# Kernel tuning notes

Measured on AMD Instinct MI355X. Metric: run time of the kernel, lower is better.

Reference implementation:

```python
import jax, jax.numpy as jnp
import numpy as np

SHAPES = ((96, 144), (48, 72), (24, 36), (12, 18))
BS, EMBED = 2, 256
HEADS, LEVELS, POINTS = 8, 4, 4
NEMBED = EMBED // HEADS
LEN_V = sum(h * w for h, w in SHAPES)
LEN_Q = LEN_V  # encoder self-attention: every pixel is a query


def _pos_grid_init():
    # Faithful re-implementation of MultiScaleDeformableAttention.pos_grid_init
    thetas = jnp.arange(HEADS, dtype=jnp.float32) * (2.0 * np.pi / HEADS)
    g = jnp.stack([jnp.cos(thetas), jnp.sin(thetas)], -1)
    g = g / jnp.max(jnp.abs(g), axis=-1, keepdims=True)
    g = jnp.tile(g.reshape(HEADS, 1, 1, 2), (1, LEVELS, POINTS, 1))
    scale = (jnp.arange(POINTS, dtype=jnp.float32) + 1.0)[None, None, :, None]
    return g * scale  # [HEADS, LEVELS, POINTS, 2]


def setup_inputs() -> dict:
    ks = jax.random.split(jax.random.key(0), 7)
    return {
        'query': jax.random.normal(ks[0], (BS, LEN_Q, EMBED), jnp.float32),
        'ref_points': jax.random.uniform(ks[1], (BS, LEN_Q, LEVELS, 2), jnp.float32),
        'value': jax.random.normal(ks[2], (BS, LEN_V, EMBED), jnp.float32),
        'pad_mask': jnp.ones((BS, LEN_V), dtype=bool),
        'value_proj_kernel': jax.random.normal(ks[3], (EMBED, HEADS, NEMBED), jnp.float32) * 0.05,
        'value_proj_bias': jnp.zeros((HEADS, NEMBED), jnp.float32),
        'sampling_offsets_kernel': jax.random.normal(ks[4], (EMBED, HEADS, LEVELS, POINTS, 2), jnp.float32) * 0.01,
        'sampling_offsets_bias': _pos_grid_init(),
        'attn_kernel': jax.random.normal(ks[5], (EMBED, HEADS, LEVELS * POINTS), jnp.float32) * 0.02,
        'attn_bias': jnp.zeros((HEADS, LEVELS * POINTS), jnp.float32),
        'out_kernel': jax.random.normal(ks[6], (HEADS, NEMBED, EMBED), jnp.float32) * 0.05,
        'out_bias': jnp.zeros((EMBED,), jnp.float32),
        'train': 0,
    }


def _bilinear(im, grid, w, h):
    """Batched 2D bilinear interpolation, zero outside the image.

    im:   [B, h*w, e] flattened feature map
    grid: [B, N, 2] normalized coords (pixel centers at (x+0.5)/w, (y+0.5)/h)
    Returns [B, N, e]. Identical math to the original gather-based kernel:
    out-of-bounds corner weights are zeroed, so zero-padding the image by 1
    reproduces the 'empty'-pad + masked-weight scheme exactly.
    """
    B, _, e = im.shape
    imp = jnp.pad(im.reshape(B, h, w, e), ((0, 0), (1, 1), (1, 1), (0, 0)))
    imp = imp.reshape(B, (h + 2) * (w + 2), e)
    x = grid[..., 0] * w - 0.5
    y = grid[..., 1] * h - 0.5
    x0 = jnp.floor(x).astype(jnp.int32)
    y0 = jnp.floor(y).astype(jnp.int32)
    x1 = x0 + 1
    y1 = y0 + 1

    def gather(yy, xx):
        idx = jnp.clip(yy + 1, 0, h + 1) * (w + 2) + jnp.clip(xx + 1, 0, w + 1)
        return jnp.take_along_axis(imp, idx[..., None], axis=1)  # [B, N, e]

    x0f, y0f = x0.astype(x.dtype), y0.astype(y.dtype)
    x1f, y1f = x1.astype(x.dtype), y1.astype(y.dtype)
    inx0 = (x0 >= 0) & (x0 <= w - 1)
    inx1 = (x1 >= 0) & (x1 <= w - 1)
    iny0 = (y0 >= 0) & (y0 <= h - 1)
    iny1 = (y1 >= 0) & (y1 <= h - 1)
    wa = jnp.where(inx0 & iny0, (x1f - x) * (y1f - y), 0.0)
    wb = jnp.where(inx0 & iny1, (x1f - x) * (y - y0f), 0.0)
    wc = jnp.where(inx1 & iny0, (x - x0f) * (y1f - y), 0.0)
    wd = jnp.where(inx1 & iny1, (x - x0f) * (y - y0f), 0.0)
    return (gather(y0, x0) * wa[..., None] + gather(y1, x0) * wb[..., None]
            + gather(y0, x1) * wc[..., None] + gather(y1, x1) * wd[..., None])


def _forward(query, ref_points, value, pad_mask, vpk, vpb, sok, sob, ak, ab, okern, obias):
    bs, len_q, _ = query.shape
    len_v = value.shape[1]
    # value projection + pad masking -> [bs*H, len_v, nembed]
    v = jnp.einsum('bve,ehd->bvhd', value, vpk) + vpb
    v = jnp.where(pad_mask[..., None, None], v, 0)
    v = v.transpose(0, 2, 1, 3).reshape(bs * HEADS, len_v, NEMBED)
    # sampling locations (ref_dim == 2 branch) -> [bs*H, L, P*len_q, 2]
    off = jnp.einsum('bqe,ehlpc->bqhlpc', query, sok) + sob
    offset_norm = jnp.array([[w, h] for h, w in SHAPES], dtype=query.dtype)  # [L, 2]
    loc = ref_points[:, :, None, :, None, :] + off / offset_norm[None, None, None, :, None, :]
    loc = loc.transpose(0, 2, 3, 4, 1, 5).reshape(bs * HEADS, LEVELS, POINTS * len_q, 2)
    # attention weights (softmax over L*P) -> [bs*H, len_q, L*P]
    aw = jnp.einsum('bqe,ehm->bqhm', query, ak) + ab
    aw = jax.nn.softmax(aw, axis=-1)
    aw = aw.transpose(0, 2, 1, 3).reshape(bs * HEADS, len_q, LEVELS * POINTS)
    # per-level bilinear sampling, concatenated level-major over (level, point)
    starts = np.cumsum([0] + [h * w for h, w in SHAPES])
    sampled = []
    for li, (h, w) in enumerate(SHAPES):
        vl = v[:, starts[li]:starts[li + 1], :]
        s = _bilinear(vl, loc[:, li], w, h)  # [bs*H, P*len_q, nembed]
        sampled.append(s.reshape(bs * HEADS, POINTS, len_q, NEMBED))
    sampled = jnp.concatenate(sampled, axis=1)  # [bs*H, L*P, len_q, nembed]
    x = jnp.einsum('blqe,bql->bqe', sampled, aw)
    x = x.reshape(bs, HEADS, len_q, NEMBED)
    # output projection: DenseGeneral over (heads, nembed)
    return jnp.einsum('bhqe,hed->bqd', x, okern) + obias


def reference(query, ref_points, value, pad_mask, value_proj_kernel, value_proj_bias,
              sampling_offsets_kernel, sampling_offsets_bias, attn_kernel, attn_bias,
              out_kernel, out_bias, train):
    del train  # eval mode (no remat); math is identical
    return _forward(query, ref_points, value, pad_mask, value_proj_kernel, value_proj_bias,
                    sampling_offsets_kernel, sampling_offsets_bias, attn_kernel, attn_bias,
                    out_kernel, out_bias)
```

## Files before the change

### kernel.cpp

```cpp
#include <hip/hip_runtime.h>
#include <math.h>

#define LEN 18360
#define M_ROWS (2 * LEN)
#define NTASK (16 * LEN)

typedef unsigned short u16;
typedef __attribute__((ext_vector_type(8))) short bf16x8;
typedef __attribute__((ext_vector_type(4))) float f32x4;

__device__ __forceinline__ u16 f2bf(float f) {
  unsigned u = __float_as_uint(f);
  return (u16)((u + 0x7fffu + ((u >> 16) & 1u)) >> 16);
}
__device__ __forceinline__ void async_cp16(const void* g, void* l) {
  __builtin_amdgcn_global_load_lds(
      (const __attribute__((address_space(1))) unsigned*)g,
      (__attribute__((address_space(3))) unsigned*)l, 16, 0, 0);
}

__global__ __launch_bounds__(256) void gemm_mfma_k(
    const u16* __restrict__ A0, const u16* __restrict__ Bt0,
    const float* __restrict__ bias0, void* __restrict__ C0, int N0, int nt0,
    int mode0, int split, const u16* __restrict__ A1,
    const u16* __restrict__ Bt1, const float* __restrict__ bias1,
    void* __restrict__ C1, int N1, int nt1, int mode1) {
  __shared__ u16 A_lds[8 * 512];
  __shared__ u16 B_lds[8 * 512];

  int bid = (int)blockIdx.x;
  const u16* A;
  const u16* Bt;
  const float* bias;
  void* Cv;
  int N, nt, mode;
  if (bid < split) {
    A = A0; Bt = Bt0; bias = bias0; Cv = C0; N = N0; nt = nt0; mode = mode0;
  } else {
    bid -= split;
    A = A1; Bt = Bt1; bias = bias1; Cv = C1; N = N1; nt = nt1; mode = mode1;
  }
  const int n0 = (bid % nt) << 7;
  const int m0 = (bid / nt) << 7;

  const int tid = threadIdx.x;
  const int w = tid >> 6;
  const int lane = tid & 63;
  const int wm = w & 1, wn = w >> 1;
  const int mr = lane & 15;
  const int kq = (lane >> 4) * 8;

  f32x4 acc[4][4];
#pragma unroll
  for (int i = 0; i < 4; i++)
#pragma unroll
    for (int j = 0; j < 4; j++) acc[i][j] = (f32x4){0.f, 0.f, 0.f, 0.f};

  for (int k0 = 0; k0 < 256; k0 += 32) {
    __syncthreads();
#pragma unroll
    for (int t = 0; t < 2; t++) {
      const int st = 2 * w + t;
      const int ga = min(m0 + st * 16 + mr, M_ROWS - 1);
      async_cp16(A + (size_t)ga * 256 + k0 + kq, &A_lds[st * 512]);
      const int gb = n0 + st * 16 + mr;
      async_cp16(Bt + (size_t)gb * 256 + k0 + kq, &B_lds[st * 512]);
    }
    __syncthreads();

    bf16x8 af[4], bf[4];
#pragma unroll
    for (int i = 0; i < 4; i++)
      af[i] = *(const bf16x8*)&A_lds[(wm * 4 + i) * 512 + lane * 8];
#pragma unroll
    for (int j = 0; j < 4; j++)
      bf[j] = *(const bf16x8*)&B_lds[(wn * 4 + j) * 512 + lane * 8];
#pragma unroll
    for (int i = 0; i < 4; i++)
#pragma unroll
      for (int j = 0; j < 4; j++)
        acc[i][j] = __builtin_amdgcn_mfma_f32_16x16x32_bf16(bf[j], af[i],
                                                            acc[i][j], 0, 0, 0);
  }

#pragma unroll
  for (int i = 0; i < 4; i++) {
    const int row = m0 + wm * 64 + i * 16 + mr;
    if (row >= M_ROWS) continue;
#pragma unroll
    for (int j = 0; j < 4; j++) {
      const int col = n0 + wn * 64 + j * 16 + (lane >> 4) * 4;
      const float4 b4 = *(const float4*)(bias + col);
      float4 o;
      o.x = acc[i][j][0] + b4.x;
      o.y = acc[i][j][1] + b4.y;
      o.z = acc[i][j][2] + b4.z;
      o.w = acc[i][j][3] + b4.w;
      if (mode == 0) {
        *(float4*)((float*)Cv + (size_t)row * N + col) = o;
      } else if (mode == 1) {
        const int b = row >= LEN;
        const int lv = row - b * LEN;
        const int h = col >> 5, d = col & 31;
        uint2 p;
        p.x = (unsigned)f2bf(o.x) | ((unsigned)f2bf(o.y) << 16);
        p.y = (unsigned)f2bf(o.z) | ((unsigned)f2bf(o.w) << 16);
        *(uint2*)((u16*)Cv + ((size_t)((b * 8 + h) * LEN + lv)) * 32 + d) = p;
      } else {
        uint2 p;
        p.x = (unsigned)f2bf(o.x) | ((unsigned)f2bf(o.y) << 16);
        p.y = (unsigned)f2bf(o.z) | ((unsigned)f2bf(o.w) << 16);
        *(uint2*)((u16*)Cv + (size_t)row * N + col) = p;
      }
    }
  }
}

__global__ __launch_bounds__(256) void cast_qv_k(const float* __restrict__ q,
                                                 const float* __restrict__ v,
                                                 u16* __restrict__ qb,
                                                 u16* __restrict__ vb) {
  const size_t i = ((size_t)blockIdx.x * 256 + threadIdx.x) * 4;
  float4 a = *(const float4*)(q + i);
  uint2 p;
  p.x = (unsigned)f2bf(a.x) | ((unsigned)f2bf(a.y) << 16);
  p.y = (unsigned)f2bf(a.z) | ((unsigned)f2bf(a.w) << 16);
  *(uint2*)&qb[i] = p;
  float4 c = *(const float4*)(v + i);
  p.x = (unsigned)f2bf(c.x) | ((unsigned)f2bf(c.y) << 16);
  p.y = (unsigned)f2bf(c.z) | ((unsigned)f2bf(c.w) << 16);
  *(uint2*)&vb[i] = p;
}

__global__ __launch_bounds__(256) void wcast_k(
    const float* __restrict__ vpk, const float* __restrict__ sok,
    const float* __restrict__ ak, const float* __restrict__ ok,
    const float* __restrict__ sob, const float* __restrict__ ab,
    u16* __restrict__ vpk_t, u16* __restrict__ sa_t, u16* __restrict__ ok_t,
    float* __restrict__ bias_cat) {
  const int gid = blockIdx.x * 256 + threadIdx.x;
  if (gid < 65536) {
    const int d = gid, n = d >> 8, k = d & 255;
    vpk_t[d] = f2bf(vpk[k * 256 + n]);
  } else if (gid < 131072) {
    const int d = gid - 65536, n = d >> 8, k = d & 255;
    sa_t[d] = f2bf(sok[k * 256 + n]);
  } else if (gid < 163840) {
    const int d = gid - 131072, n = d >> 8, k = d & 255;
    sa_t[65536 + d] = f2bf(ak[k * 128 + n]);
  } else if (gid < 229376) {
    const int d = gid - 163840, n = d >> 8, k = d & 255;
    ok_t[d] = f2bf(ok[k * 256 + n]);
  } else if (gid < 229760) {
    const int d = gid - 229376;
    bias_cat[d] = (d < 256) ? sob[d] : ab[d - 256];
  }
}

__global__ __launch_bounds__(256) void sampler_k(
    const u16* __restrict__ v,
    const u16* __restrict__ offaw,
    const float* __restrict__ refp,
    u16* __restrict__ xb)
{
  __shared__ int2 meta[4][258];
  const int tid = threadIdx.x;

  const int cW[4] = {144, 72, 36, 18};
  const int cH[4] = {96, 48, 24, 12};
  const int cS[4] = {0, 13824, 17280, 18144};

  {
    const int t = tid >> 4;
    const int s = tid & 15;
    const int l = s >> 2;

    const int task = (blockIdx.x << 4) + t;
    const int q = task % LEN;
    const int bh = task / LEN;
    const int h = bh & 7;
    const int b = bh >> 3;
    const size_t qrow = (size_t)(b * LEN + q);
    const u16* rowp = offaw + qrow * 384;

    const float logit = __uint_as_float((unsigned)rowp[256 + h * 16 + s] << 16);
    float mx = logit;
#pragma unroll
    for (int m = 1; m < 16; m <<= 1) mx = fmaxf(mx, __shfl_xor(mx, m, 16));
    const float e = __expf(logit - mx);
    float ssum = e;
#pragma unroll
    for (int m = 1; m < 16; m <<= 1) ssum += __shfl_xor(ssum, m, 16);
    const float wsm = e / ssum;

    const int W = cW[l], H = cH[l], ST = cS[l];
    const float2 rp = ((const float2*)(refp + qrow * 8))[l];
    const unsigned upair = ((const unsigned*)(rowp + h * 32))[s];
    const float ox = __uint_as_float(upair << 16);
    const float oy = __uint_as_float(upair & 0xffff0000u);
    const float X = rp.x * (float)W + ox - 0.5f;
    const float Y = rp.y * (float)H + oy - 0.5f;
    const float fx = floorf(X), fy = floorf(Y);
    const int x0 = (int)fx, y0 = (int)fy;
    const float dx = X - fx, dy = Y - fy;
    const float ux = 1.f - dx, uy = 1.f - dy;
    const bool bx0 = (unsigned)x0 < (unsigned)W;
    const bool bx1 = (unsigned)(x0 + 1) < (unsigned)W;
    const bool by0 = (unsigned)y0 < (unsigned)H;
    const bool by1 = (unsigned)(y0 + 1) < (unsigned)H;
    const int xc0 = min(max(x0, 0), W - 1);
    const int xc1 = min(max(x0 + 1, 0), W - 1);
    const int yc0 = min(max(y0, 0), H - 1);
    const int yc1 = min(max(y0 + 1, 0), H - 1);
    const float w00 = (bx0 & by0) ? wsm * ux * uy : 0.f;
    const float w10 = (bx1 & by0) ? wsm * dx * uy : 0.f;
    const float w01 = (bx0 & by1) ? wsm * ux * dy : 0.f;
    const float w11 = (bx1 & by1) ? wsm * dx * dy : 0.f;

    meta[0][tid] = make_int2((ST + yc0 * W + xc0) << 6, __float_as_int(w00));
    meta[1][tid] = make_int2((ST + yc0 * W + xc1) << 6, __float_as_int(w10));
    meta[2][tid] = make_int2((ST + yc1 * W + xc0) << 6, __float_as_int(w01));
    meta[3][tid] = make_int2((ST + yc1 * W + xc1) << 6, __float_as_int(w11));
  }
  __syncthreads();

  const int u = tid >> 5;
  const int lane = tid & 31;
  const int c = lane >> 3;
  const int dq = lane & 7;

#pragma unroll
  for (int rep = 0; rep < 2; rep++) {
    const int t = u + rep * 8;
    const int task = (blockIdx.x << 4) + t;
    const int q = task % LEN;
    const int bh = task / LEN;
    const int h = bh & 7;
    const int b = bh >> 3;
    const size_t qrow = (size_t)(b * LEN + q);
    const char* vb = (const char*)v + (size_t)bh * LEN * 64;

    float4 acc = make_float4(0.f, 0.f, 0.f, 0.f);
#pragma unroll
    for (int s = 0; s < 16; s++) {
      const int2 m2 = meta[c][t * 16 + s];
      const float wgt = __int_as_float(m2.y);
      const uint2 pv = *(const uint2*)(vb + (size_t)(unsigned)m2.x + (dq << 3));
      acc.x = fmaf(wgt, __uint_as_float(pv.x << 16), acc.x);
      acc.y = fmaf(wgt, __uint_as_float(pv.x & 0xffff0000u), acc.y);
      acc.z = fmaf(wgt, __uint_as_float(pv.y << 16), acc.z);
      acc.w = fmaf(wgt, __uint_as_float(pv.y & 0xffff0000u), acc.w);
    }
#pragma unroll
    for (int m = 8; m <= 16; m <<= 1) {
      acc.x += __shfl_xor(acc.x, m, 32);
      acc.y += __shfl_xor(acc.y, m, 32);
      acc.z += __shfl_xor(acc.z, m, 32);
      acc.w += __shfl_xor(acc.w, m, 32);
    }
    if (c == 0) {
      uint2 p;
      p.x = (unsigned)f2bf(acc.x) | ((unsigned)f2bf(acc.y) << 16);
      p.y = (unsigned)f2bf(acc.z) | ((unsigned)f2bf(acc.w) << 16);
      *(uint2*)&xb[qrow * 256 + h * 32 + (dq << 2)] = p;
    }
  }
}

extern "C" void kernel_launch(void* const* d_in, const int* in_sizes, int n_in,
                              void* d_out, int out_size, void* d_ws,
                              size_t ws_size, hipStream_t stream) {
  (void)in_sizes; (void)n_in; (void)out_size; (void)ws_size;

  const float* query = (const float*)d_in[0];
  const float* refp = (const float*)d_in[1];
  const float* value = (const float*)d_in[2];
  const float* vpk = (const float*)d_in[4];
  const float* vpb = (const float*)d_in[5];
  const float* sok = (const float*)d_in[6];
  const float* sob = (const float*)d_in[7];
  const float* ak = (const float*)d_in[8];
  const float* ab = (const float*)d_in[9];
  const float* okern = (const float*)d_in[10];
  const float* obias = (const float*)d_in[11];

  char* p = (char*)d_ws;
  u16* v_ws = (u16*)p;   p += (size_t)M_ROWS * 256 * 2;
  u16* offaw = (u16*)p;  p += (size_t)M_ROWS * 384 * 2;
  u16* qbf = (u16*)p;    p += (size_t)M_ROWS * 256 * 2;
  u16* vbf = (u16*)p;    p += (size_t)M_ROWS * 256 * 2;
  u16* vpk_t = (u16*)p;  p += 65536 * 2;
  u16* sa_t = (u16*)p;   p += 98304 * 2;
  u16* ok_t = (u16*)p;   p += 65536 * 2;
  float* bias_cat = (float*)p;
  u16* x_b = qbf;

  const dim3 blk(256);
  const int mt = (M_ROWS + 127) / 128;

  cast_qv_k<<<dim3(2350080 / 256), blk, 0, stream>>>(query, value, qbf, vbf);
  wcast_k<<<dim3(898), blk, 0, stream>>>(vpk, sok, ak, okern, sob, ab, vpk_t,
                                         sa_t, ok_t, bias_cat);
  gemm_mfma_k<<<dim3(2 * mt + 3 * mt), blk, 0, stream>>>(
      vbf, vpk_t, vpb, v_ws, 256, 2, 1, 2 * mt,
      qbf, sa_t, bias_cat, offaw, 384, 3, 2);
  sampler_k<<<dim3(NTASK / 16), blk, 0, stream>>>(v_ws, offaw, refp, x_b);
  gemm_mfma_k<<<dim3(2 * mt), blk, 0, stream>>>(
      x_b, ok_t, obias, (float*)d_out, 256, 2, 0, 2 * mt,
      x_b, ok_t, obias, (float*)d_out, 256, 2, 0);
}
```

Before: 274.6 us.

## Restructure sampler: 32 tasks per block, 16-byte gathers, packed FMA

The deformable-attention sampler now handles 32 query-head tasks per block instead of 16. Each task uses 8 threads instead of 32, and each thread gathers 16 bytes (8 bf16 channels) per corner instead of 8 bytes, accumulating two corners with packed float2 FMAs. This halves the cross-lane reduction and widens the output stores. The metadata layout is padded to avoid LDS bank conflicts and the level constants are computed arithmetically. In exchange, per-thread gather parallelism drops and the number of blocks is halved, which may reduce latency hiding.

```diff
diff --git a/kernel.cpp b/kernel.cpp
--- a/kernel.cpp
+++ b/kernel.cpp
@@ -8,6 +8,7 @@
 typedef unsigned short u16;
 typedef __attribute__((ext_vector_type(8))) short bf16x8;
 typedef __attribute__((ext_vector_type(4))) float f32x4;
+typedef __attribute__((ext_vector_type(2))) float f32x2;
 
 __device__ __forceinline__ u16 f2bf(float f) {
   unsigned u = __float_as_uint(f);
@@ -17,6 +18,9 @@
   __builtin_amdgcn_global_load_lds(
       (const __attribute__((address_space(1))) unsigned*)g,
       (__attribute__((address_space(3))) unsigned*)l, 16, 0, 0);
+}
+__device__ __forceinline__ f32x2 bfpair(unsigned u) {
+  return (f32x2){__uint_as_float(u << 16), __uint_as_float(u & 0xffff0000u)};
 }
 
 __global__ __launch_bounds__(256) void gemm_mfma_k(
@@ -163,19 +167,16 @@
     const float* __restrict__ refp,
     u16* __restrict__ xb)
 {
-  __shared__ int2 meta[4][258];
+  __shared__ int2 meta[4 * 552];
   const int tid = threadIdx.x;
 
-  const int cW[4] = {144, 72, 36, 18};
-  const int cH[4] = {96, 48, 24, 12};
-  const int cS[4] = {0, 13824, 17280, 18144};
-
-  {
-    const int t = tid >> 4;
+#pragma unroll
+  for (int rep = 0; rep < 2; rep++) {
+    const int t = rep * 16 + (tid >> 4);
     const int s = tid & 15;
     const int l = s >> 2;
 
-    const int task = (blockIdx.x << 4) + t;
+    const int task = (blockIdx.x << 5) + t;
     const int q = task % LEN;
     const int bh = task / LEN;
     const int h = bh & 7;
@@ -193,7 +194,8 @@
     for (int m = 1; m < 16; m <<= 1) ssum += __shfl_xor(ssum, m, 16);
     const float wsm = e / ssum;
 
-    const int W = cW[l], H = cH[l], ST = cS[l];
+    const int W = 144 >> l, H = 96 >> l;
+    const int ST = 18432 - (18432 >> (2 * l));
     const float2 rp = ((const float2*)(refp + qrow * 8))[l];
     const unsigned upair = ((const unsigned*)(rowp + h * 32))[s];
     const float ox = __uint_as_float(upair << 16);
@@ -217,53 +219,63 @@
     const float w01 = (bx0 & by1) ? wsm * ux * dy : 0.f;
     const float w11 = (bx1 & by1) ? wsm * dx * dy : 0.f;
 
-    meta[0][tid] = make_int2((ST + yc0 * W + xc0) << 6, __float_as_int(w00));
-    meta[1][tid] = make_int2((ST + yc0 * W + xc1) << 6, __float_as_int(w10));
-    meta[2][tid] = make_int2((ST + yc1 * W + xc0) << 6, __float_as_int(w01));
-    meta[3][tid] = make_int2((ST + yc1 * W + xc1) << 6, __float_as_int(w11));
+    int2* mt = &meta[t * 17 + s];
+    mt[0 * 552] = make_int2((ST + yc0 * W + xc0) << 6, __float_as_int(w00));
+    mt[1 * 552] = make_int2((ST + yc0 * W + xc1) << 6, __float_as_int(w10));
+    mt[2 * 552] = make_int2((ST + yc1 * W + xc0) << 6, __float_as_int(w01));
+    mt[3 * 552] = make_int2((ST + yc1 * W + xc1) << 6, __float_as_int(w11));
   }
   __syncthreads();
 
-  const int u = tid >> 5;
-  const int lane = tid & 31;
-  const int c = lane >> 3;
-  const int dq = lane & 7;
-
-#pragma unroll
-  for (int rep = 0; rep < 2; rep++) {
-    const int t = u + rep * 8;
-    const int task = (blockIdx.x << 4) + t;
-    const int q = task % LEN;
-    const int bh = task / LEN;
-    const int h = bh & 7;
-    const int b = bh >> 3;
-    const size_t qrow = (size_t)(b * LEN + q);
-    const char* vb = (const char*)v + (size_t)bh * LEN * 64;
-
-    float4 acc = make_float4(0.f, 0.f, 0.f, 0.f);
+  const int u = tid >> 3;
+  const int c2 = (tid >> 2) & 1;
+  const int dq = tid & 3;
+
+  const int task = (blockIdx.x << 5) + u;
+  const int q = task % LEN;
+  const int bh = task / LEN;
+  const int h = bh & 7;
+  const int b = bh >> 3;
+  const size_t qrow = (size_t)(b * LEN + q);
+  const char* vb = (const char*)v +
+                   (size_t)__builtin_amdgcn_readfirstlane(bh) * (LEN * 64);
+  const int dqo = dq << 4;
+
+  f32x2 a0 = {0.f, 0.f}, a1 = {0.f, 0.f}, a2 = {0.f, 0.f}, a3 = {0.f, 0.f};
+#pragma unroll
+  for (int ci = 0; ci < 2; ci++) {
+    const int2* mrow = &meta[(c2 + 2 * ci) * 552 + u * 17];
 #pragma unroll
     for (int s = 0; s < 16; s++) {
-      const int2 m2 = meta[c][t * 16 + s];
+      const int2 m2 = mrow[s];
       const float wgt = __int_as_float(m2.y);
-      const uint2 pv = *(const uint2*)(vb + (size_t)(unsigned)m2.x + (dq << 3));
-      acc.x = fmaf(wgt, __uint_as_float(pv.x << 16), acc.x);
-      acc.y = fmaf(wgt, __uint_as_float(pv.x & 0xffff0000u), acc.y);
-      acc.z = fmaf(wgt, __uint_as_float(pv.y << 16), acc.z);
-      acc.w = fmaf(wgt, __uint_as_float(pv.y & 0xffff0000u), acc.w);
+      const f32x2 wp = {wgt, wgt};
+      const uint4 pv = *(const uint4*)(vb + (unsigned)m2.x + dqo);
+#if __has_builtin(__builtin_elementwise_fma)
+      a0 = __builtin_elementwise_fma(wp, bfpair(pv.x), a0);
+      a1 = __builtin_elementwise_fma(wp, bfpair(pv.y), a1);
+      a2 = __builtin_elementwise_fma(wp, bfpair(pv.z), a2);
+      a3 = __builtin_elementwise_fma(wp, bfpair(pv.w), a3);
+#else
+      a0 = wp * bfpair(pv.x) + a0;
+      a1 = wp * bfpair(pv.y) + a1;
+      a2 = wp * bfpair(pv.z) + a2;
+      a3 = wp * bfpair(pv.w) + a3;
+#endif
     }
-#pragma unroll
-    for (int m = 8; m <= 16; m <<= 1) {
-      acc.x += __shfl_xor(acc.x, m, 32);
-      acc.y += __shfl_xor(acc.y, m, 32);
-      acc.z += __shfl_xor(acc.z, m, 32);
-      acc.w += __shfl_xor(acc.w, m, 32);
-    }
-    if (c == 0) {
-      uint2 p;
-      p.x = (unsigned)f2bf(acc.x) | ((unsigned)f2bf(acc.y) << 16);
-      p.y = (unsigned)f2bf(acc.z) | ((unsigned)f2bf(acc.w) << 16);
-      *(uint2*)&xb[qrow * 256 + h * 32 + (dq << 2)] = p;
-    }
+  }
+  a0.x += __shfl_xor(a0.x, 4); a0.y += __shfl_xor(a0.y, 4);
+  a1.x += __shfl_xor(a1.x, 4); a1.y += __shfl_xor(a1.y, 4);
+  a2.x += __shfl_xor(a2.x, 4); a2.y += __shfl_xor(a2.y, 4);
+  a3.x += __shfl_xor(a3.x, 4); a3.y += __shfl_xor(a3.y, 4);
+
+  if (c2 == 0) {
+    uint4 o;
+    o.x = (unsigned)f2bf(a0.x) | ((unsigned)f2bf(a0.y) << 16);
+    o.y = (unsigned)f2bf(a1.x) | ((unsigned)f2bf(a1.y) << 16);
+    o.z = (unsigned)f2bf(a2.x) | ((unsigned)f2bf(a2.y) << 16);
+    o.w = (unsigned)f2bf(a3.x) | ((unsigned)f2bf(a3.y) << 16);
+    *(uint4*)&xb[qrow * 256 + h * 32 + (dq << 3)] = o;
   }
 }
 
@@ -304,7 +316,7 @@
   gemm_mfma_k<<<dim3(2 * mt + 3 * mt), blk, 0, stream>>>(
       vbf, vpk_t, vpb, v_ws, 256, 2, 1, 2 * mt,
       qbf, sa_t, bias_cat, offaw, 384, 3, 2);
-  sampler_k<<<dim3(NTASK / 16), blk, 0, stream>>>(v_ws, offaw, refp, x_b);
+  sampler_k<<<dim3(NTASK / 32), blk, 0, stream>>>(v_ws, offaw, refp, x_b);
   gemm_mfma_k<<<dim3(2 * mt), blk, 0, stream>>>(
       x_b, ok_t, obias, (float*)d_out, 256, 2, 0, 2 * mt,
       x_b, ok_t, obias, (float*)d_out, 256, 2, 0);
```

Result: faster. 260.4 us (-5.2%).
